# Kernel tuning notes

Hardware: AMD Instinct MI355X
Metric: run time of the kernel (lower is better)

The kernel has to match this reference:

```python
import jax, jax.numpy as jnp
import numpy as np

E = 128
H = 4
D = E // H  # head dim = 32
NEG = -1e9


def setup_inputs() -> dict:
    key = jax.random.key(0)
    ks = jax.random.split(key, 4)
    B, N = 8, 2048
    x = jax.random.normal(ks[0], (B, N, E), dtype=jnp.float32)
    adj = jax.random.randint(ks[1], (B, N, N), 0, 2, dtype=jnp.int32)
    # nn.MultiheadAttention params: packed in_proj (3E,E) + out_proj (E,E)
    in_proj_w = jax.random.normal(ks[2], (3 * E, E), dtype=jnp.float32) * (1.0 / np.sqrt(E))
    in_proj_b = jnp.zeros((3 * E,), dtype=jnp.float32)
    out_w = jax.random.normal(ks[3], (E, E), dtype=jnp.float32) * (1.0 / np.sqrt(E))
    out_b = jnp.zeros((E,), dtype=jnp.float32)
    return {"x": x, "adj": adj, "in_proj_w": in_proj_w, "in_proj_b": in_proj_b,
            "out_w": out_w, "out_b": out_b}


def reference(x, adj, in_proj_w, in_proj_b, out_w, out_b):
    B, N, _ = x.shape
    # additive mask from FIRST batch element only (as in the torch module)
    mask = jnp.where(adj[0] == 0, jnp.float32(NEG), jnp.float32(0.0))  # (N,N)
    # packed QKV projection: x @ W^T + b
    qkv = x @ in_proj_w.T + in_proj_b  # (B,N,3E)
    q, k, v = jnp.split(qkv, 3, axis=-1)
    # (B,N,E) -> (B,H,N,D)
    def heads(t):
        return t.reshape(B, N, H, D).transpose(0, 2, 1, 3)
    q, k, v = heads(q), heads(k), heads(v)
    scores = jnp.einsum('bhnd,bhmd->bhnm', q, k) / jnp.sqrt(jnp.float32(D))
    scores = scores + mask[None, None]  # broadcast shared mask
    attn = jax.nn.softmax(scores, axis=-1)
    out = jnp.einsum('bhnm,bhmd->bhnd', attn, v)  # (B,H,N,D)
    out = out.transpose(0, 2, 1, 3).reshape(B, N, E)
    return out @ out_w.T + out_b
```

## Files before the change

### kernel.cpp

```cpp
#include <hip/hip_runtime.h>


#define EDIM 128
#define SCALE2 0.25503483f
#define COFF  -5.7707801f

typedef unsigned int uint32;
typedef float f32x4 __attribute__((ext_vector_type(4)));
typedef short s16x8 __attribute__((ext_vector_type(8)));
typedef _Float16 f16x2 __attribute__((ext_vector_type(2)));
typedef _Float16 f16x4 __attribute__((ext_vector_type(4)));
typedef _Float16 f16x8 __attribute__((ext_vector_type(8)));
typedef __fp16 g16x2 __attribute__((ext_vector_type(2)));

__device__ inline float bf2f(ushort u) { return __uint_as_float(((uint32)u) << 16); }
__device__ inline ushort f2bf(float f) {
  uint32 u = __float_as_uint(f);
  u += 0x7fffu + ((u >> 16) & 1u);
  return (ushort)(u >> 16);
}
__device__ inline uint32 packbf(float a, float b) {
  uint32 ua = __float_as_uint(a) + 0x8000u;
  uint32 ub = __float_as_uint(b) + 0x8000u;
  return __builtin_amdgcn_perm(ub, ua, 0x07060302u);
}
__device__ inline f16x2 pkrtz(float a, float b) {
  g16x2 t = __builtin_amdgcn_cvt_pkrtz(a, b);
  return __builtin_bit_cast(f16x2, t);
}
__device__ inline float fexp2(float x) {
#if __has_builtin(__builtin_amdgcn_exp2f)
  return __builtin_amdgcn_exp2f(x);
#else
  return __exp2f(x);
#endif
}

__device__ inline f32x4 mfma32(s16x8 a, s16x8 b, f32x4 c) {
  return __builtin_amdgcn_mfma_f32_16x16x32_bf16(a, b, c, 0, 0, 0);
}
__device__ inline f32x4 mfma32h(f16x8 a, f16x8 b, f32x4 c) {
  return __builtin_amdgcn_mfma_f32_16x16x32_f16(a, b, c, 0, 0, 0);
}

__device__ inline int sniff_fp32(const ushort* __restrict__ xus) {
  int lane = threadIdx.x & 63, cnt = 0;
#pragma unroll
  for (int i = 0; i < 4; i++) {
    ushort v = xus[2 * (lane * 4 + i)];
    int ex = (v >> 7) & 0xFF;
    cnt += (ex >= 100 && ex <= 140) ? 1 : 0;
  }
#pragma unroll
  for (int s = 1; s < 64; s <<= 1) cnt += __shfl_xor(cnt, s);
  return cnt < 128;
}

__device__ inline s16x8 load8(const void* p, size_t e, int fp32) {
  if (fp32) {
    const float* f = (const float*)p + e;
    float4 lo = *(const float4*)f;
    float4 hi = *(const float4*)(f + 4);
    union { s16x8 s; uint32 u[4]; } r;
    r.u[0] = packbf(lo.x, lo.y);
    r.u[1] = packbf(lo.z, lo.w);
    r.u[2] = packbf(hi.x, hi.y);
    r.u[3] = packbf(hi.z, hi.w);
    return r.s;
  }
  return *(const s16x8*)((const ushort*)p + e);
}
__device__ inline float loads(const void* p, size_t e, int fp32) {
  return fp32 ? ((const float*)p)[e] : bf2f(((const ushort*)p)[e]);
}

__global__ __launch_bounds__(256) void k_pre(const void* __restrict__ x,
                                             const void* __restrict__ w,
                                             const void* __restrict__ bias,
                                             ushort* __restrict__ Qg,
                                             ushort* __restrict__ Kg,
                                             _Float16* __restrict__ Vth,
                                             const int4* __restrict__ adj4,
                                             uint32* __restrict__ mb) {
  if (blockIdx.y >= 6) {
    int g = ((blockIdx.y - 6) * 256 + blockIdx.x) * 256 + threadIdx.x;
    int4 v = adj4[g];
    int lane = threadIdx.x & 63;
    uint32 nib = (v.x != 0 ? 1u : 0u) | (v.y != 0 ? 2u : 0u) |
                 (v.z != 0 ? 4u : 0u) | (v.w != 0 ? 8u : 0u);
    uint32 wbit = nib << (4 * (lane & 7));
    wbit |= __shfl_xor(wbit, 1);
    wbit |= __shfl_xor(wbit, 2);
    wbit |= __shfl_xor(wbit, 4);
    if ((lane & 7) == 0) mb[g >> 3] = wbit;
    return;
  }

  const int fp32 = sniff_fp32((const ushort*)x);
  const int tid = threadIdx.x;
  const int wave = tid >> 6, lane = tid & 63, L = lane & 15, quad = lane >> 4;
  const int mt = blockIdx.x * 64 + wave * 16;
  const int jt0 = blockIdx.y * 4;

  s16x8 a[4];
#pragma unroll
  for (int ks = 0; ks < 4; ks++)
    a[ks] = load8(x, (size_t)(mt + L) * EDIM + ks * 32 + quad * 8, fp32);

  const int bidx = mt >> 11;
  const int npos0 = (mt & 2047) + quad * 4;

  for (int jj = 0; jj < 4; jj++) {
    int jt = jt0 + jj;
    f32x4 acc = {0.f, 0.f, 0.f, 0.f};
#pragma unroll
    for (int ks = 0; ks < 4; ks++) {
      s16x8 bf = load8(w, (size_t)(jt * 16 + L) * EDIM + ks * 32 + quad * 8, fp32);
      acc = mfma32(a[ks], bf, acc);
    }
    int j = jt * 16 + L;
    float badd = loads(bias, j, fp32);
    int jm = j & 127;
    int h = jm >> 5, d = jm & 31;
    int bh = bidx * 4 + h;
    int ch = npos0 >> 7, kk = npos0 & 127;
    if (jt < 8) {
#pragma unroll
      for (int r = 0; r < 4; r++)
        Qg[(size_t)bh * 65536 + (size_t)(npos0 + r) * 32 + d] = f2bf((acc[r] + badd) * SCALE2);
    } else if (jt < 16) {
      int sub = kk >> 5, k32 = kk & 31, t = k32 >> 3, r8 = k32 & 7;
      int slot0 = sub * 32 + ((r8 >> 2) << 4) + t * 4;
      size_t kb = (size_t)bh * 65536 + (size_t)ch * 4096;
#pragma unroll
      for (int r = 0; r < 4; r++)
        Kg[kb + (size_t)(slot0 + r) * 32 + (((d >> 3) ^ r) << 3) + (d & 7)] =
            f2bf(acc[r] + badd);
    } else {
      int g = kk >> 3, e0 = kk & 7;
      f16x2 h0 = pkrtz(acc[0] + badd, acc[1] + badd);
      f16x2 h1 = pkrtz(acc[2] + badd, acc[3] + badd);
      f16x4 pk; pk[0] = h0[0]; pk[1] = h0[1]; pk[2] = h1[0]; pk[3] = h1[1];
      *(f16x4*)(Vth + (size_t)bh * 65536 + (size_t)ch * 4096 + d * 128 +
                (g ^ (d & 7)) * 8 + e0) = pk;
    }
  }
}

__global__ __launch_bounds__(512, 4) void k_attn(const ushort* __restrict__ Qg,
                                                 const ushort* __restrict__ Kg,
                                                 const _Float16* __restrict__ Vth,
                                                 const uint32* __restrict__ mb,
                                                 ushort* __restrict__ Oa) {
  __shared__ float cb[4352];

  const int tid = threadIdx.x;
  const int wv = tid >> 6, lane = tid & 63, L = lane & 15, quad = lane >> 4;
  const int half = wv >> 2, wl = wv & 3;
  const int bh = blockIdx.x >> 4;
  const int q0 = (blockIdx.x & 15) * 128 + wl * 32;
  const int qgA = q0 + L, qgB = q0 + 16 + L;

  const ushort* Qb = Qg + (size_t)bh * 65536;
  s16x8 qfA = *(const s16x8*)(Qb + (size_t)qgA * 32 + quad * 8);
  s16x8 qfB = *(const s16x8*)(Qb + (size_t)qgB * 32 + quad * 8);

  f32x4 OA0 = {0,0,0,0}, OA1 = {0,0,0,0}, OB0 = {0,0,0,0}, OB1 = {0,0,0,0};
  f32x4 LA = {0,0,0,0}, LB = {0,0,0,0};
  f16x8 ones;
#pragma unroll
  for (int i = 0; i < 8; i++) ones[i] = (_Float16)1.0f;

  const char* Kg8 = (const char*)(Kg + (size_t)bh * 65536) + (size_t)half * 65536;
  const char* Vg8 = (const char*)(Vth + (size_t)bh * 65536) + (size_t)half * 65536;
  const int g0 = quad ^ (L & 3);

  const char* kA = Kg8 + L * 64 + g0 * 16;
  const char* vA = Vg8 + L * 256;

  for (int cc = 0; cc < 8; cc++) {
    const int c = half * 8 + cc;
    uint4 mA = *(const uint4*)(mb + (size_t)qgA * 64 + c * 4);
    uint4 mB = *(const uint4*)(mb + (size_t)qgB * 64 + c * 4);
    uint32 mAw[4] = {mA.x, mA.y, mA.z, mA.w};
    uint32 mBw[4] = {mB.x, mB.y, mB.z, mB.w};
    const char* kc = kA + (size_t)cc * 8192;
    const char* vc = vA + (size_t)cc * 8192;

#pragma unroll
    for (int sub = 0; sub < 4; sub++) {
      const f32x4 Zc = {COFF, COFF, COFF, COFF};
      s16x8 kf0 = *(const s16x8*)(kc + sub * 2048);
      s16x8 kf1 = *(const s16x8*)(kc + sub * 2048 + 1024);
      f32x4 sA0 = mfma32(kf0, qfA, Zc), sA1 = mfma32(kf1, qfA, Zc);
      f32x4 sB0 = mfma32(kf0, qfB, Zc), sB1 = mfma32(kf1, qfB, Zc);

      uint32 mwqA = mAw[sub] >> (quad * 8);
      uint32 mwqB = mBw[sub] >> (quad * 8);
      union { f16x8 v; f16x2 h[4]; } pA, pB;
      float a0 = ((mwqA >> 0) & 1u) ? fexp2(sA0[0]) : 0.f;
      float a1 = ((mwqA >> 1) & 1u) ? fexp2(sA0[1]) : 0.f;
      float a2 = ((mwqA >> 2) & 1u) ? fexp2(sA0[2]) : 0.f;
      float a3 = ((mwqA >> 3) & 1u) ? fexp2(sA0[3]) : 0.f;
      float a4 = ((mwqA >> 4) & 1u) ? fexp2(sA1[0]) : 0.f;
      float a5 = ((mwqA >> 5) & 1u) ? fexp2(sA1[1]) : 0.f;
      float a6 = ((mwqA >> 6) & 1u) ? fexp2(sA1[2]) : 0.f;
      float a7 = ((mwqA >> 7) & 1u) ? fexp2(sA1[3]) : 0.f;
      pA.h[0] = pkrtz(a0, a1); pA.h[1] = pkrtz(a2, a3);
      pA.h[2] = pkrtz(a4, a5); pA.h[3] = pkrtz(a6, a7);
      float b0 = ((mwqB >> 0) & 1u) ? fexp2(sB0[0]) : 0.f;
      float b1 = ((mwqB >> 1) & 1u) ? fexp2(sB0[1]) : 0.f;
      float b2 = ((mwqB >> 2) & 1u) ? fexp2(sB0[2]) : 0.f;
      float b3 = ((mwqB >> 3) & 1u) ? fexp2(sB0[3]) : 0.f;
      float b4 = ((mwqB >> 4) & 1u) ? fexp2(sB1[0]) : 0.f;
      float b5 = ((mwqB >> 5) & 1u) ? fexp2(sB1[1]) : 0.f;
      float b6 = ((mwqB >> 6) & 1u) ? fexp2(sB1[2]) : 0.f;
      float b7 = ((mwqB >> 7) & 1u) ? fexp2(sB1[3]) : 0.f;
      pB.h[0] = pkrtz(b0, b1); pB.h[1] = pkrtz(b2, b3);
      pB.h[2] = pkrtz(b4, b5); pB.h[3] = pkrtz(b6, b7);

      int g = (sub * 4 + quad) ^ (L & 7);
      f16x8 vf0 = *(const f16x8*)(vc + g * 16);
      f16x8 vf1 = *(const f16x8*)(vc + 4096 + g * 16);
      OA0 = mfma32h(vf0, pA.v, OA0);  OA1 = mfma32h(vf1, pA.v, OA1);
      OB0 = mfma32h(vf0, pB.v, OB0);  OB1 = mfma32h(vf1, pB.v, OB1);
      LA  = mfma32h(ones, pA.v, LA);  LB  = mfma32h(ones, pB.v, LB);
    }
  }

  __syncthreads();
  const int cbase = wl * 1088;
  if (half) {
#pragma unroll
    for (int r = 0; r < 4; r++) {
      cb[cbase + L * 33 + quad * 4 + r]             = OA0[r];
      cb[cbase + L * 33 + 16 + quad * 4 + r]        = OA1[r];
      cb[cbase + (16 + L) * 33 + quad * 4 + r]      = OB0[r];
      cb[cbase + (16 + L) * 33 + 16 + quad * 4 + r] = OB1[r];
    }
    if (quad == 0) {
      cb[cbase + 1056 + L]      = LA[0];
      cb[cbase + 1056 + 16 + L] = LB[0];
    }
  }
  __syncthreads();
  if (!half) {
#pragma unroll
    for (int r = 0; r < 4; r++) {
      OA0[r] += cb[cbase + L * 33 + quad * 4 + r];
      OA1[r] += cb[cbase + L * 33 + 16 + quad * 4 + r];
      OB0[r] += cb[cbase + (16 + L) * 33 + quad * 4 + r];
      OB1[r] += cb[cbase + (16 + L) * 33 + 16 + quad * 4 + r];
    }
    float rnA = 1.0f / (LA[0] + cb[cbase + 1056 + L]);
    float rnB = 1.0f / (LB[0] + cb[cbase + 1056 + 16 + L]);
    int b = bh >> 2, h = bh & 3;
    {
      size_t ob = ((size_t)(b * 2048 + qgA)) * 128 + h * 32 + quad * 4;
      ushort4 p0, p1;
      p0.x = f2bf(OA0[0] * rnA); p0.y = f2bf(OA0[1] * rnA);
      p0.z = f2bf(OA0[2] * rnA); p0.w = f2bf(OA0[3] * rnA);
      p1.x = f2bf(OA1[0] * rnA); p1.y = f2bf(OA1[1] * rnA);
      p1.z = f2bf(OA1[2] * rnA); p1.w = f2bf(OA1[3] * rnA);
      *(ushort4*)(Oa + ob) = p0; *(ushort4*)(Oa + ob + 16) = p1;
    }
    {
      size_t ob = ((size_t)(b * 2048 + qgB)) * 128 + h * 32 + quad * 4;
      ushort4 p0, p1;
      p0.x = f2bf(OB0[0] * rnB); p0.y = f2bf(OB0[1] * rnB);
      p0.z = f2bf(OB0[2] * rnB); p0.w = f2bf(OB0[3] * rnB);
      p1.x = f2bf(OB1[0] * rnB); p1.y = f2bf(OB1[1] * rnB);
      p1.z = f2bf(OB1[2] * rnB); p1.w = f2bf(OB1[3] * rnB);
      *(ushort4*)(Oa + ob) = p0; *(ushort4*)(Oa + ob + 16) = p1;
    }
  }
}

__global__ __launch_bounds__(256) void k_proj(void* outp, const ushort* Oa,
                                              const void* w, const void* bias,
                                              const ushort* __restrict__ xus) {
  const int fp32 = sniff_fp32(xus);
  const ushort* src = Oa;
  const int tid = threadIdx.x;
  const int wave = tid >> 6, lane = tid & 63, L = lane & 15, quad = lane >> 4;
  const int mt = blockIdx.x * 64 + wave * 16;
  const int jt0 = blockIdx.y * 2;

  s16x8 a[4];
#pragma unroll
  for (int ks = 0; ks < 4; ks++)
    a[ks] = *(const s16x8*)(src + (size_t)(mt + L) * EDIM + ks * 32 + quad * 8);

  for (int jt = jt0; jt < jt0 + 2; jt++) {
    f32x4 acc = {0.f, 0.f, 0.f, 0.f};
#pragma unroll
    for (int ks = 0; ks < 4; ks++) {
      s16x8 bf = load8(w, (size_t)(jt * 16 + L) * EDIM + ks * 32 + quad * 8, fp32);
      acc = mfma32(a[ks], bf, acc);
    }
    float badd = loads(bias, jt * 16 + L, fp32);
#pragma unroll
    for (int r = 0; r < 4; r++) {
      size_t idx = (size_t)(mt + quad * 4 + r) * EDIM + jt * 16 + L;
      if (fp32) ((float*)outp)[idx] = acc[r] + badd;
      else      ((ushort*)outp)[idx] = f2bf(acc[r] + badd);
    }
  }
}

extern "C" void kernel_launch(void* const* d_in, const int* in_sizes, int n_in,
                              void* d_out, int out_size, void* d_ws, size_t ws_size,
                              hipStream_t stream) {
  const void* x   = d_in[0];
  const int*  adj = (const int*)d_in[1];
  const void* ipw = d_in[2];
  const void* ipb = d_in[3];
  const void* ow  = d_in[4];
  const void* ob  = d_in[5];

  char* ws = (char*)d_ws;
  ushort*   Qg  = (ushort*)(ws);
  ushort*   Kg  = (ushort*)(ws + ((size_t)4 << 20));
  _Float16* Vth = (_Float16*)(ws + ((size_t)8 << 20));
  uint32*   mb  = (uint32*)(ws + ((size_t)12 << 20));
  ushort*   Oa  = (ushort*)(ws + ((size_t)13 << 20));

  hipLaunchKernelGGL(k_pre, dim3(256, 22), dim3(256), 0, stream, x, ipw, ipb,
                     Qg, Kg, Vth, (const int4*)adj, mb);
  hipLaunchKernelGGL(k_attn, dim3(512), dim3(512), 0, stream, Qg, Kg, Vth, mb,
                     Oa);
  hipLaunchKernelGGL(k_proj, dim3(256, 4), dim3(256), 0, stream, d_out, Oa, ow, ob,
                     (const ushort*)x);
}
```

Baseline: 248.4 us.

## Halve per-wave query rows in attention, double grid, remap blocks for K/V locality

Each wave of the attention kernel now handles 16 query rows instead of 32, so the grid doubles to 1024 blocks of 64 queries. Launch bounds rise to 8 blocks per SM and the shared reduction buffer shrinks to match. Block IDs are remapped so consecutive blocks cover different batch-heads at the same query chunk, and the chunk loop is fully unrolled. The aim is more waves in flight to hide K/V load latency, at the cost of loading each K/V fragment for fewer query rows, which doubles K/V traffic per query.

Measured after the change: 258.7 us. 4.2% more time.

```diff
diff --git a/kernel.cpp b/kernel.cpp
--- a/kernel.cpp
+++ b/kernel.cpp
@@ -147,26 +147,26 @@
   }
 }
 
-__global__ __launch_bounds__(512, 4) void k_attn(const ushort* __restrict__ Qg,
+__global__ __launch_bounds__(512, 8) void k_attn(const ushort* __restrict__ Qg,
                                                  const ushort* __restrict__ Kg,
                                                  const _Float16* __restrict__ Vth,
                                                  const uint32* __restrict__ mb,
                                                  ushort* __restrict__ Oa) {
-  __shared__ float cb[4352];
+  __shared__ float cb[2176];
 
   const int tid = threadIdx.x;
   const int wv = tid >> 6, lane = tid & 63, L = lane & 15, quad = lane >> 4;
   const int half = wv >> 2, wl = wv & 3;
-  const int bh = blockIdx.x >> 4;
-  const int q0 = (blockIdx.x & 15) * 128 + wl * 32;
-  const int qgA = q0 + L, qgB = q0 + 16 + L;
+  const int bid = blockIdx.x;
+  const int bh = ((bid >> 3) & 3) * 8 + (bid & 7);
+  const int qc = bid >> 5;
+  const int q0 = qc * 64 + wl * 16;
+  const int qgA = q0 + L;
 
   const ushort* Qb = Qg + (size_t)bh * 65536;
   s16x8 qfA = *(const s16x8*)(Qb + (size_t)qgA * 32 + quad * 8);
-  s16x8 qfB = *(const s16x8*)(Qb + (size_t)qgB * 32 + quad * 8);
-
-  f32x4 OA0 = {0,0,0,0}, OA1 = {0,0,0,0}, OB0 = {0,0,0,0}, OB1 = {0,0,0,0};
-  f32x4 LA = {0,0,0,0}, LB = {0,0,0,0};
+
+  f32x4 OA0 = {0,0,0,0}, OA1 = {0,0,0,0}, LA = {0,0,0,0};
   f16x8 ones;
 #pragma unroll
   for (int i = 0; i < 8; i++) ones[i] = (_Float16)1.0f;
@@ -177,27 +177,24 @@
 
   const char* kA = Kg8 + L * 64 + g0 * 16;
   const char* vA = Vg8 + L * 256;
-
+  const uint32* mbA = mb + (size_t)qgA * 64 + half * 32;
+
+#define MW4(M, S) ((S) == 0 ? (M).x : (S) == 1 ? (M).y : (S) == 2 ? (M).z : (M).w)
+
+#pragma unroll
   for (int cc = 0; cc < 8; cc++) {
-    const int c = half * 8 + cc;
-    uint4 mA = *(const uint4*)(mb + (size_t)qgA * 64 + c * 4);
-    uint4 mB = *(const uint4*)(mb + (size_t)qgB * 64 + c * 4);
-    uint32 mAw[4] = {mA.x, mA.y, mA.z, mA.w};
-    uint32 mBw[4] = {mB.x, mB.y, mB.z, mB.w};
-    const char* kc = kA + (size_t)cc * 8192;
-    const char* vc = vA + (size_t)cc * 8192;
-
+    uint4 mA = *(const uint4*)(mbA + cc * 4);
+    const char* kc = kA + cc * 8192;
+    const char* vc = vA + cc * 8192;
 #pragma unroll
     for (int sub = 0; sub < 4; sub++) {
       const f32x4 Zc = {COFF, COFF, COFF, COFF};
       s16x8 kf0 = *(const s16x8*)(kc + sub * 2048);
       s16x8 kf1 = *(const s16x8*)(kc + sub * 2048 + 1024);
       f32x4 sA0 = mfma32(kf0, qfA, Zc), sA1 = mfma32(kf1, qfA, Zc);
-      f32x4 sB0 = mfma32(kf0, qfB, Zc), sB1 = mfma32(kf1, qfB, Zc);
-
-      uint32 mwqA = mAw[sub] >> (quad * 8);
-      uint32 mwqB = mBw[sub] >> (quad * 8);
-      union { f16x8 v; f16x2 h[4]; } pA, pB;
+
+      uint32 mwqA = MW4(mA, sub) >> (quad * 8);
+      union { f16x8 v; f16x2 h[4]; } pA;
       float a0 = ((mwqA >> 0) & 1u) ? fexp2(sA0[0]) : 0.f;
       float a1 = ((mwqA >> 1) & 1u) ? fexp2(sA0[1]) : 0.f;
       float a2 = ((mwqA >> 2) & 1u) ? fexp2(sA0[2]) : 0.f;
@@ -208,40 +205,26 @@
       float a7 = ((mwqA >> 7) & 1u) ? fexp2(sA1[3]) : 0.f;
       pA.h[0] = pkrtz(a0, a1); pA.h[1] = pkrtz(a2, a3);
       pA.h[2] = pkrtz(a4, a5); pA.h[3] = pkrtz(a6, a7);
-      float b0 = ((mwqB >> 0) & 1u) ? fexp2(sB0[0]) : 0.f;
-      float b1 = ((mwqB >> 1) & 1u) ? fexp2(sB0[1]) : 0.f;
-      float b2 = ((mwqB >> 2) & 1u) ? fexp2(sB0[2]) : 0.f;
-      float b3 = ((mwqB >> 3) & 1u) ? fexp2(sB0[3]) : 0.f;
-      float b4 = ((mwqB >> 4) & 1u) ? fexp2(sB1[0]) : 0.f;
-      float b5 = ((mwqB >> 5) & 1u) ? fexp2(sB1[1]) : 0.f;
-      float b6 = ((mwqB >> 6) & 1u) ? fexp2(sB1[2]) : 0.f;
-      float b7 = ((mwqB >> 7) & 1u) ? fexp2(sB1[3]) : 0.f;
-      pB.h[0] = pkrtz(b0, b1); pB.h[1] = pkrtz(b2, b3);
-      pB.h[2] = pkrtz(b4, b5); pB.h[3] = pkrtz(b6, b7);
-
-      int g = (sub * 4 + quad) ^ (L & 7);
-      f16x8 vf0 = *(const f16x8*)(vc + g * 16);
-      f16x8 vf1 = *(const f16x8*)(vc + 4096 + g * 16);
-      OA0 = mfma32h(vf0, pA.v, OA0);  OA1 = mfma32h(vf1, pA.v, OA1);
-      OB0 = mfma32h(vf0, pB.v, OB0);  OB1 = mfma32h(vf1, pB.v, OB1);
-      LA  = mfma32h(ones, pA.v, LA);  LB  = mfma32h(ones, pB.v, LB);
-    }
-  }
+
+      int vg = (sub * 4 + quad) ^ (L & 7);
+      f16x8 vf0 = *(const f16x8*)(vc + vg * 16);
+      f16x8 vf1 = *(const f16x8*)(vc + 4096 + vg * 16);
+      OA0 = mfma32h(vf0, pA.v, OA0);
+      OA1 = mfma32h(vf1, pA.v, OA1);
+      LA  = mfma32h(ones, pA.v, LA);
+    }
+  }
+#undef MW4
 
   __syncthreads();
-  const int cbase = wl * 1088;
+  const int cbase = wl * 544;
   if (half) {
 #pragma unroll
     for (int r = 0; r < 4; r++) {
-      cb[cbase + L * 33 + quad * 4 + r]             = OA0[r];
-      cb[cbase + L * 33 + 16 + quad * 4 + r]        = OA1[r];
-      cb[cbase + (16 + L) * 33 + quad * 4 + r]      = OB0[r];
-      cb[cbase + (16 + L) * 33 + 16 + quad * 4 + r] = OB1[r];
-    }
-    if (quad == 0) {
-      cb[cbase + 1056 + L]      = LA[0];
-      cb[cbase + 1056 + 16 + L] = LB[0];
-    }
+      cb[cbase + L * 33 + quad * 4 + r]      = OA0[r];
+      cb[cbase + L * 33 + 16 + quad * 4 + r] = OA1[r];
+    }
+    if (quad == 0) cb[cbase + 528 + L] = LA[0];
   }
   __syncthreads();
   if (!half) {
@@ -249,30 +232,16 @@
     for (int r = 0; r < 4; r++) {
       OA0[r] += cb[cbase + L * 33 + quad * 4 + r];
       OA1[r] += cb[cbase + L * 33 + 16 + quad * 4 + r];
-      OB0[r] += cb[cbase + (16 + L) * 33 + quad * 4 + r];
-      OB1[r] += cb[cbase + (16 + L) * 33 + 16 + quad * 4 + r];
-    }
-    float rnA = 1.0f / (LA[0] + cb[cbase + 1056 + L]);
-    float rnB = 1.0f / (LB[0] + cb[cbase + 1056 + 16 + L]);
+    }
+    float rn = 1.0f / (LA[0] + cb[cbase + 528 + L]);
     int b = bh >> 2, h = bh & 3;
-    {
-      size_t ob = ((size_t)(b * 2048 + qgA)) * 128 + h * 32 + quad * 4;
-      ushort4 p0, p1;
-      p0.x = f2bf(OA0[0] * rnA); p0.y = f2bf(OA0[1] * rnA);
-      p0.z = f2bf(OA0[2] * rnA); p0.w = f2bf(OA0[3] * rnA);
-      p1.x = f2bf(OA1[0] * rnA); p1.y = f2bf(OA1[1] * rnA);
-      p1.z = f2bf(OA1[2] * rnA); p1.w = f2bf(OA1[3] * rnA);
-      *(ushort4*)(Oa + ob) = p0; *(ushort4*)(Oa + ob + 16) = p1;
-    }
-    {
-      size_t ob = ((size_t)(b * 2048 + qgB)) * 128 + h * 32 + quad * 4;
-      ushort4 p0, p1;
-      p0.x = f2bf(OB0[0] * rnB); p0.y = f2bf(OB0[1] * rnB);
-      p0.z = f2bf(OB0[2] * rnB); p0.w = f2bf(OB0[3] * rnB);
-      p1.x = f2bf(OB1[0] * rnB); p1.y = f2bf(OB1[1] * rnB);
-      p1.z = f2bf(OB1[2] * rnB); p1.w = f2bf(OB1[3] * rnB);
-      *(ushort4*)(Oa + ob) = p0; *(ushort4*)(Oa + ob + 16) = p1;
-    }
+    size_t ob = ((size_t)(b * 2048 + qgA)) * 128 + h * 32 + quad * 4;
+    ushort4 p0, p1;
+    p0.x = f2bf(OA0[0] * rn); p0.y = f2bf(OA0[1] * rn);
+    p0.z = f2bf(OA0[2] * rn); p0.w = f2bf(OA0[3] * rn);
+    p1.x = f2bf(OA1[0] * rn); p1.y = f2bf(OA1[1] * rn);
+    p1.z = f2bf(OA1[2] * rn); p1.w = f2bf(OA1[3] * rn);
+    *(ushort4*)(Oa + ob) = p0; *(ushort4*)(Oa + ob + 16) = p1;
   }
 }
 
@@ -327,7 +296,7 @@
 
   hipLaunchKernelGGL(k_pre, dim3(256, 22), dim3(256), 0, stream, x, ipw, ipb,
                      Qg, Kg, Vth, (const int4*)adj, mb);
-  hipLaunchKernelGGL(k_attn, dim3(512), dim3(512), 0, stream, Qg, Kg, Vth, mb,
+  hipLaunchKernelGGL(k_attn, dim3(1024), dim3(512), 0, stream, Qg, Kg, Vth, mb,
                      Oa);
   hipLaunchKernelGGL(k_proj, dim3(256, 4), dim3(256), 0, stream, d_out, Oa, ow, ob,
                      (const ushort*)x);
```
